# Kernel optimization log

Measured on AMD Instinct MI355X. Metric: run time of the kernel, lower is better.

Reference implementation:

```python
import jax, jax.numpy as jnp
import numpy as np

NUM_HEADS = 6
WS = 3

def setup_inputs() -> dict:
    key = jax.random.key(0)
    k1, k2, k3 = jax.random.split(key, 3)
    dim = 192
    x = jax.random.normal(k1, (2, dim, 48, 48, 48), dtype=jnp.float32)
    Wqkv = jax.random.normal(k2, (3 * dim, dim), dtype=jnp.float32) * (dim ** -0.5)
    Wproj = jax.random.normal(k3, (dim, dim), dtype=jnp.float32) * (dim ** -0.5)
    bproj = jnp.zeros((dim,), dtype=jnp.float32)
    return {"x": x, "Wqkv": Wqkv, "Wproj": Wproj, "bproj": bproj, "H": 384, "W": 288}

def reference(x, Wqkv, Wproj, bproj, H, W):
    b, c, h, w, d = x.shape
    xt = x.reshape(b, -1, c)                      # (B, N, C) with C = c, N = h*w*d
    B, N, C = xt.shape
    nh, ws = NUM_HEADS, WS
    hd = C // nh
    scale = hd ** -0.5
    hg, wg = H // ws, W // ws
    tg = hg * wg
    # window partition: (B, hg, ws, wg, ws, C) -> (B, hg, wg, ws, ws, C)
    xw = xt.reshape(B, hg, ws, wg, ws, C).transpose(0, 1, 3, 2, 4, 5)
    # fused QKV projection (no bias)
    qkv = jnp.einsum('bgvijc,oc->bgvijo', xw, Wqkv)          # (B,hg,wg,ws,ws,3C)
    qkv = qkv.reshape(B, tg, ws * ws, 3, nh, hd).transpose(3, 0, 1, 4, 2, 5)
    q, k, v = qkv[0], qkv[1], qkv[2]                          # (B, tg, nh, 9, hd)
    attn = jnp.einsum('bgnqd,bgnkd->bgnqk', q, k) * scale     # (B, tg, nh, 9, 9)
    attn = jax.nn.softmax(attn, axis=-1)
    out = jnp.einsum('bgnqk,bgnkd->bgnqd', attn, v)           # (B, tg, nh, 9, hd)
    out = out.transpose(0, 1, 3, 2, 4).reshape(B, hg, wg, ws, ws, C)
    out = jnp.swapaxes(out, 2, 3).reshape(B, N, C)            # un-window
    out = out @ Wproj.T + bproj
    return out.reshape(b, c, h, w, d)
```

## Files before the change

kernel.cpp:

```cpp
#include <hip/hip_runtime.h>

typedef _Float16 f16;
typedef _Float16 f16x4 __attribute__((ext_vector_type(4)));
typedef _Float16 f16x8 __attribute__((ext_vector_type(8)));
typedef float f32x4 __attribute__((ext_vector_type(4)));

#define TPB  576
#define NWIN 16
#define XS   200
#define WSS  200
#define QS   40
#define VS   264

#define WSQF_HALVES 110592
#define WS_NEEDED   (221184 + 73728)

__global__ __launch_bounds__(512) void conv_w(
    const float* __restrict__ Wqkv, const float* __restrict__ Wproj,
    f16* __restrict__ wsWqf, f16* __restrict__ wsWpf)
{
    int idx = blockIdx.x * 512 + threadIdx.x;
    if (idx < WSQF_HALVES) {
        int h    = idx / 18432;
        int rem  = idx % 18432;
        int ct   = rem / 3072;
        int rem2 = rem % 3072;
        int kk   = rem2 / 512;
        int rem3 = rem2 % 512;
        int lane = rem3 / 8;
        int e    = rem3 % 8;
        int r    = 16 * ct + (lane & 15);
        int grow = (r >> 5) * 192 + h * 32 + (r & 31);
        int col  = kk * 32 + (lane >> 4) * 8 + e;
        wsWqf[idx] = (f16)Wqkv[grow * 192 + col];
    } else {
        int j    = idx - WSQF_HALVES;
        int h    = j / 6144;
        int rem  = j % 6144;
        int nt   = rem / 512;
        int rem2 = rem % 512;
        int lane = rem2 / 8;
        int e    = rem2 % 8;
        wsWpf[j] = (f16)Wproj[(16 * nt + (lane & 15)) * 192 + h * 32 + (lane >> 4) * 8 + e];
    }
}

__global__ __launch_bounds__(TPB) void lsa_mfma11(
    const float* __restrict__ x, const f16* __restrict__ wsWqf,
    const f16* __restrict__ wsWpf, const float* __restrict__ bproj,
    float* __restrict__ out)
{
    __shared__ __attribute__((aligned(16))) f16 Xh[144 * XS];
    __shared__ __attribute__((aligned(16))) f16 Qh[144 * QS];
    __shared__ __attribute__((aligned(16))) f16 Kh[144 * QS];
    __shared__ __attribute__((aligned(16))) f16 Vt2[32 * VS];
    __shared__ __attribute__((aligned(16))) f16 AOh[144 * QS];

    const int tid  = threadIdx.x;
    const int lane = tid & 63;
    const int w    = tid >> 6;
    const int ci   = w / 3;
    const int ti   = w % 3;
    const int l15  = lane & 15;
    const int lg   = lane >> 4;

    const int  bb    = blockIdx.x / 768;
    const int  gbase = (blockIdx.x % 768) * NWIN;
    const long rb0   = (long)bb * 110592 + (long)(gbase / 96) * 864 + (long)(gbase % 96) * 3;

    const f16x8* wqf = (const f16x8*)wsWqf;
    const f16x8* wpf = (const f16x8*)wsWpf;

    for (int idx = tid; idx < 144 * 48; idx += TPB) {
        int t = idx / 48, c4 = idx % 48;
        int wi = t / 9, q = t - 9 * wi;
        long grow = rb0 + wi * 3 + (q / 3) * 288 + (q % 3);
        float4 xv = ((const float4*)x)[grow * 48 + c4];
        union { f16 h[4]; ushort4 u; } tmp;
        tmp.h[0] = (f16)xv.x; tmp.h[1] = (f16)xv.y; tmp.h[2] = (f16)xv.z; tmp.h[3] = (f16)xv.w;
        *(ushort4*)&Xh[t * XS + c4 * 4] = tmp.u;
    }
    {
        int4 z = {0, 0, 0, 0};
        for (int i2 = tid; i2 < (32 * VS * 2) / 16; i2 += TPB) ((int4*)Vt2)[i2] = z;
    }

    f32x4 pacc[3][4];
    #pragma unroll
    for (int a = 0; a < 3; ++a)
        #pragma unroll
        for (int bq = 0; bq < 4; ++bq)
            pacc[a][bq] = (f32x4){0.f, 0.f, 0.f, 0.f};

    __syncthreads();

    for (int h = 0; h < 6; ++h) {
        f32x4 qacc[2][3];
        #pragma unroll
        for (int c = 0; c < 2; ++c)
            #pragma unroll
            for (int t = 0; t < 3; ++t)
                qacc[c][t] = (f32x4){0.f, 0.f, 0.f, 0.f};
        #pragma unroll
        for (int kk = 0; kk < 6; ++kk) {
            f16x8 af[2], bf[3];
            af[0] = wqf[((h * 6 + ci    ) * 6 + kk) * 64 + lane];
            af[1] = wqf[((h * 6 + ci + 3) * 6 + kk) * 64 + lane];
            #pragma unroll
            for (int t = 0; t < 3; ++t)
                bf[t] = *(const f16x8*)&Xh[(16 * (ti + 3 * t) + l15) * XS + kk * 32 + lg * 8];
            #pragma unroll
            for (int c = 0; c < 2; ++c)
                #pragma unroll
                for (int t = 0; t < 3; ++t)
                    qacc[c][t] = __builtin_amdgcn_mfma_f32_16x16x32_f16(af[c], bf[t], qacc[c][t], 0, 0, 0);
        }
        #pragma unroll
        for (int c = 0; c < 2; ++c) {
            const int ct = ci + 3 * c;
            #pragma unroll
            for (int t = 0; t < 3; ++t) {
                const int token = 16 * (ti + 3 * t) + l15;
                f16x4 ph;
                ph[0] = (f16)qacc[c][t][0]; ph[1] = (f16)qacc[c][t][1];
                ph[2] = (f16)qacc[c][t][2]; ph[3] = (f16)qacc[c][t][3];
                if (ct < 2) {
                    *(f16x4*)&Qh[token * QS + ct * 16 + 4 * lg] = ph;
                } else if (ct < 4) {
                    *(f16x4*)&Kh[token * QS + (ct - 2) * 16 + 4 * lg] = ph;
                } else {
                    const int d0 = (ct - 4) * 16 + 4 * lg;
                    int wi = token / 9, qq = token - 9 * wi;
                    #pragma unroll
                    for (int r = 0; r < 4; ++r)
                        Vt2[(d0 + r) * VS + 16 * wi + qq] = ph[r];
                }
            }
        }
        __syncthreads();

        for (int wi = w; wi < NWIN; wi += 9) {
            int krow = 9 * wi + l15;
            krow = krow > 143 ? 143 : krow;
            f16x8 ak = *(const f16x8*)&Kh[krow * QS + lg * 8];
            f16x8 aq = *(const f16x8*)&Qh[krow * QS + lg * 8];
            f32x4 s = (f32x4){0.f, 0.f, 0.f, 0.f};
            s = __builtin_amdgcn_mfma_f32_16x16x32_f16(ak, aq, s, 0, 0, 0);
            float lgt[4];
            float mx = -1e30f;
            #pragma unroll
            for (int r = 0; r < 4; ++r) {
                int kx = 4 * lg + r;
                lgt[r] = (kx < 9) ? s[r] * 0.17677669529663687f : -1e30f;
                mx = fmaxf(mx, lgt[r]);
            }
            mx = fmaxf(mx, __shfl_xor(mx, 16));
            mx = fmaxf(mx, __shfl_xor(mx, 32));
            float e[4], sum = 0.f;
            #pragma unroll
            for (int r = 0; r < 4; ++r) {
                int kx = 4 * lg + r;
                e[r] = (kx < 9) ? __expf(lgt[r] - mx) : 0.f;
                sum += e[r];
            }
            sum += __shfl_xor(sum, 16);
            sum += __shfl_xor(sum, 32);
            float inv = 1.0f / sum;
            f16x4 p;
            p[0] = (f16)(e[0] * inv); p[1] = (f16)(e[1] * inv);
            p[2] = (f16)(e[2] * inv); p[3] = (f16)(e[3] * inv);
            #pragma unroll
            for (int dt = 0; dt < 2; ++dt) {
                f16x4 av = *(const f16x4*)&Vt2[(dt * 16 + l15) * VS + 16 * wi + 4 * lg];
                f32x4 o = (f32x4){0.f, 0.f, 0.f, 0.f};
                o = __builtin_amdgcn_mfma_f32_16x16x16f16(av, p, o, 0, 0, 0);
                if (l15 < 9) {
                    f16x4 oh;
                    oh[0] = (f16)o[0]; oh[1] = (f16)o[1]; oh[2] = (f16)o[2]; oh[3] = (f16)o[3];
                    *(f16x4*)&AOh[(9 * wi + l15) * QS + dt * 16 + 4 * lg] = oh;
                }
            }
        }
        __syncthreads();

        {
            f16x8 bw[4];
            #pragma unroll
            for (int bq = 0; bq < 4; ++bq)
                bw[bq] = wpf[(h * 12 + 4 * ti + bq) * 64 + lane];
            f16x8 aof[3];
            #pragma unroll
            for (int a = 0; a < 3; ++a)
                aof[a] = *(const f16x8*)&AOh[(16 * (3 * ci + a) + l15) * QS + lg * 8];
            #pragma unroll
            for (int bq = 0; bq < 4; ++bq)
                #pragma unroll
                for (int a = 0; a < 3; ++a)
                    pacc[a][bq] = __builtin_amdgcn_mfma_f32_16x16x32_f16(aof[a], bw[bq], pacc[a][bq], 0, 0, 0);
        }
    }

    float bv[4];
    #pragma unroll
    for (int bq = 0; bq < 4; ++bq)
        bv[bq] = bproj[16 * (4 * ti + bq) + l15];
    #pragma unroll
    for (int a = 0; a < 3; ++a) {
        #pragma unroll
        for (int r = 0; r < 4; ++r) {
            int t = 16 * (3 * ci + a) + lg * 4 + r;
            int wi = t / 9, q = t - 9 * wi;
            long grow = rb0 + wi * 3 + (q / 3) * 288 + (q % 3);
            float* dst = out + grow * 192;
            #pragma unroll
            for (int bq = 0; bq < 4; ++bq)
                dst[16 * (4 * ti + bq) + l15] = pacc[a][bq][r] + bv[bq];
        }
    }
}

__global__ __launch_bounds__(TPB) void lsa_mfma7(
    const float* __restrict__ x, const float* __restrict__ Wqkv,
    const float* __restrict__ Wproj, const float* __restrict__ bproj,
    float* __restrict__ out)
{
    __shared__ f16 Xh[144 * XS];
    __shared__ f16 Wh[96 * WSS];
    __shared__ f16 Qh[144 * QS];
    __shared__ f16 Kh[144 * QS];
    __shared__ f16 Vt2[32 * VS];
    __shared__ f16 AOh[144 * QS];
    __shared__ f16 Wp[192 * QS];

    const int tid  = threadIdx.x;
    const int lane = tid & 63;
    const int w    = tid >> 6;
    const int ci   = w / 3;
    const int ti   = w % 3;
    const int l15  = lane & 15;
    const int lg   = lane >> 4;

    const int  bb    = blockIdx.x / 768;
    const int  gbase = (blockIdx.x % 768) * NWIN;
    const long rb0   = (long)bb * 110592 + (long)(gbase / 96) * 864 + (long)(gbase % 96) * 3;

    const float4* Wq4 = (const float4*)Wqkv;
    const float4* Wp4 = (const float4*)Wproj;

    for (int idx = tid; idx < 144 * 48; idx += TPB) {
        int t = idx / 48, c4 = idx % 48;
        int wi = t / 9, q = t - 9 * wi;
        long grow = rb0 + wi * 3 + (q / 3) * 288 + (q % 3);
        float4 xv = ((const float4*)x)[grow * 48 + c4];
        union { f16 h[4]; ushort4 u; } tmp;
        tmp.h[0] = (f16)xv.x; tmp.h[1] = (f16)xv.y; tmp.h[2] = (f16)xv.z; tmp.h[3] = (f16)xv.w;
        *(ushort4*)&Xh[t * XS + c4 * 4] = tmp.u;
    }
    {
        int4 z = {0, 0, 0, 0};
        for (int i2 = tid; i2 < (32 * VS * 2) / 16; i2 += TPB) ((int4*)Vt2)[i2] = z;
    }
    #pragma unroll
    for (int i = 0; i < 8; ++i) {
        int l = i * TPB + tid;
        int r = l / 48, c4 = l % 48;
        float4 wv = Wq4[((r >> 5) * 192 + (r & 31)) * 48 + c4];
        union { f16 h4[4]; ushort4 u; } t;
        t.h4[0] = (f16)wv.x; t.h4[1] = (f16)wv.y; t.h4[2] = (f16)wv.z; t.h4[3] = (f16)wv.w;
        *(ushort4*)&Wh[r * WSS + c4 * 4] = t.u;
    }

    f32x4 pacc[3][4];
    #pragma unroll
    for (int a = 0; a < 3; ++a)
        #pragma unroll
        for (int bq = 0; bq < 4; ++bq)
            pacc[a][bq] = (f32x4){0.f, 0.f, 0.f, 0.f};

    __syncthreads();

    for (int h = 0; h < 6; ++h) {
        f32x4 qacc[2][3];
        #pragma unroll
        for (int c = 0; c < 2; ++c)
            #pragma unroll
            for (int t = 0; t < 3; ++t)
                qacc[c][t] = (f32x4){0.f, 0.f, 0.f, 0.f};
        #pragma unroll
        for (int kk = 0; kk < 6; ++kk) {
            f16x8 af[2], bf[3];
            #pragma unroll
            for (int c = 0; c < 2; ++c)
                af[c] = *(const f16x8*)&Wh[(16 * (ci + 3 * c) + l15) * WSS + kk * 32 + lg * 8];
            #pragma unroll
            for (int t = 0; t < 3; ++t)
                bf[t] = *(const f16x8*)&Xh[(16 * (ti + 3 * t) + l15) * XS + kk * 32 + lg * 8];
            #pragma unroll
            for (int c = 0; c < 2; ++c)
                #pragma unroll
                for (int t = 0; t < 3; ++t)
                    qacc[c][t] = __builtin_amdgcn_mfma_f32_16x16x32_f16(af[c], bf[t], qacc[c][t], 0, 0, 0);
        }
        #pragma unroll
        for (int c = 0; c < 2; ++c) {
            const int ct = ci + 3 * c;
            #pragma unroll
            for (int t = 0; t < 3; ++t) {
                const int token = 16 * (ti + 3 * t) + l15;
                f16x4 ph;
                ph[0] = (f16)qacc[c][t][0]; ph[1] = (f16)qacc[c][t][1];
                ph[2] = (f16)qacc[c][t][2]; ph[3] = (f16)qacc[c][t][3];
                if (ct < 2) {
                    *(f16x4*)&Qh[token * QS + ct * 16 + 4 * lg] = ph;
                } else if (ct < 4) {
                    *(f16x4*)&Kh[token * QS + (ct - 2) * 16 + 4 * lg] = ph;
                } else {
                    const int d0 = (ct - 4) * 16 + 4 * lg;
                    int wi = token / 9, qq = token - 9 * wi;
                    #pragma unroll
                    for (int r = 0; r < 4; ++r)
                        Vt2[(d0 + r) * VS + 16 * wi + qq] = ph[r];
                }
            }
        }
        __syncthreads();

        float4 wpv[3];
        if (tid < 512) {
            #pragma unroll
            for (int i = 0; i < 3; ++i) {
                int l = i * 512 + tid;
                int r = l / 8, c4 = l % 8;
                wpv[i] = Wp4[r * 48 + h * 8 + c4];
            }
        }
        if (h < 5) {
            #pragma unroll
            for (int i = 0; i < 8; ++i) {
                int l = i * TPB + tid;
                int r = l / 48, c4 = l % 48;
                float4 wv = Wq4[((r >> 5) * 192 + (h + 1) * 32 + (r & 31)) * 48 + c4];
                union { f16 h4[4]; ushort4 u; } t;
                t.h4[0] = (f16)wv.x; t.h4[1] = (f16)wv.y; t.h4[2] = (f16)wv.z; t.h4[3] = (f16)wv.w;
                *(ushort4*)&Wh[r * WSS + c4 * 4] = t.u;
            }
        }
        for (int wi = w; wi < NWIN; wi += 9) {
            int krow = 9 * wi + l15;
            krow = krow > 143 ? 143 : krow;
            f16x8 ak = *(const f16x8*)&Kh[krow * QS + lg * 8];
            f16x8 aq = *(const f16x8*)&Qh[krow * QS + lg * 8];
            f32x4 s = (f32x4){0.f, 0.f, 0.f, 0.f};
            s = __builtin_amdgcn_mfma_f32_16x16x32_f16(ak, aq, s, 0, 0, 0);
            float lgt[4];
            float mx = -1e30f;
            #pragma unroll
            for (int r = 0; r < 4; ++r) {
                int kx = 4 * lg + r;
                lgt[r] = (kx < 9) ? s[r] * 0.17677669529663687f : -1e30f;
                mx = fmaxf(mx, lgt[r]);
            }
            mx = fmaxf(mx, __shfl_xor(mx, 16));
            mx = fmaxf(mx, __shfl_xor(mx, 32));
            float e[4], sum = 0.f;
            #pragma unroll
            for (int r = 0; r < 4; ++r) {
                int kx = 4 * lg + r;
                e[r] = (kx < 9) ? __expf(lgt[r] - mx) : 0.f;
                sum += e[r];
            }
            sum += __shfl_xor(sum, 16);
            sum += __shfl_xor(sum, 32);
            float inv = 1.0f / sum;
            f16x4 p;
            p[0] = (f16)(e[0] * inv); p[1] = (f16)(e[1] * inv);
            p[2] = (f16)(e[2] * inv); p[3] = (f16)(e[3] * inv);
            #pragma unroll
            for (int dt = 0; dt < 2; ++dt) {
                f16x4 av = *(const f16x4*)&Vt2[(dt * 16 + l15) * VS + 16 * wi + 4 * lg];
                f32x4 o = (f32x4){0.f, 0.f, 0.f, 0.f};
                o = __builtin_amdgcn_mfma_f32_16x16x16f16(av, p, o, 0, 0, 0);
                if (l15 < 9) {
                    f16x4 oh;
                    oh[0] = (f16)o[0]; oh[1] = (f16)o[1]; oh[2] = (f16)o[2]; oh[3] = (f16)o[3];
                    *(f16x4*)&AOh[(9 * wi + l15) * QS + dt * 16 + 4 * lg] = oh;
                }
            }
        }
        if (tid < 512) {
            #pragma unroll
            for (int i = 0; i < 3; ++i) {
                int l = i * 512 + tid;
                int r = l / 8, c4 = l % 8;
                union { f16 h4[4]; ushort4 u; } t;
                t.h4[0] = (f16)wpv[i].x; t.h4[1] = (f16)wpv[i].y;
                t.h4[2] = (f16)wpv[i].z; t.h4[3] = (f16)wpv[i].w;
                *(ushort4*)&Wp[r * QS + c4 * 4] = t.u;
            }
        }
        __syncthreads();

        {
            f16x8 aof[3];
            #pragma unroll
            for (int a = 0; a < 3; ++a)
                aof[a] = *(const f16x8*)&AOh[(16 * (3 * ci + a) + l15) * QS + lg * 8];
            #pragma unroll
            for (int bq = 0; bq < 4; ++bq) {
                f16x8 bw = *(const f16x8*)&Wp[(16 * (4 * ti + bq) + l15) * QS + lg * 8];
                #pragma unroll
                for (int a = 0; a < 3; ++a)
                    pacc[a][bq] = __builtin_amdgcn_mfma_f32_16x16x32_f16(aof[a], bw, pacc[a][bq], 0, 0, 0);
            }
        }
    }

    float bv[4];
    #pragma unroll
    for (int bq = 0; bq < 4; ++bq)
        bv[bq] = bproj[16 * (4 * ti + bq) + l15];
    #pragma unroll
    for (int a = 0; a < 3; ++a) {
        #pragma unroll
        for (int r = 0; r < 4; ++r) {
            int t = 16 * (3 * ci + a) + lg * 4 + r;
            int wi = t / 9, q = t - 9 * wi;
            long grow = rb0 + wi * 3 + (q / 3) * 288 + (q % 3);
            float* dst = out + grow * 192;
            #pragma unroll
            for (int bq = 0; bq < 4; ++bq)
                dst[16 * (4 * ti + bq) + l15] = pacc[a][bq][r] + bv[bq];
        }
    }
}

extern "C" void kernel_launch(void* const* d_in, const int* in_sizes, int n_in,
                              void* d_out, int out_size, void* d_ws, size_t ws_size,
                              hipStream_t stream) {
    const float* x     = (const float*)d_in[0];
    const float* Wqkv  = (const float*)d_in[1];
    const float* Wproj = (const float*)d_in[2];
    const float* bproj = (const float*)d_in[3];
    float* out = (float*)d_out;
    if (ws_size >= (size_t)WS_NEEDED && d_ws != nullptr) {
        f16* wsWqf = (f16*)d_ws;
        f16* wsWpf = (f16*)((char*)d_ws + 221184);
        conv_w<<<288, 512, 0, stream>>>(Wqkv, Wproj, wsWqf, wsWpf);
        lsa_mfma11<<<1536, TPB, 0, stream>>>(x, wsWqf, wsWpf, bproj, out);
    } else {
        lsa_mfma7<<<1536, TPB, 0, stream>>>(x, Wqkv, Wproj, bproj, out);
    }
}
```

Baseline: 227.9 us.

## Process two heads per phase with double-buffered Q/K/V/AO to halve barriers

The fused windowed-attention kernel now computes QKV for two heads before each barrier, storing into duplicated shared buffers, then runs attention for 32 window-head items and two projection accumulations per phase. This halves the number of block-wide barriers and lets warps share attention work across heads. It raises LDS usage substantially and changes the V transpose stride from 264 to 260, which alters bank mapping. The fallback kernel gets its own V stride constant.

```diff
diff --git a/kernel.cpp b/kernel.cpp
--- a/kernel.cpp
+++ b/kernel.cpp
@@ -10,7 +10,8 @@
 #define XS   200
 #define WSS  200
 #define QS   40
-#define VS   264
+#define VS   260
+#define VSF  264
 
 #define WSQF_HALVES 110592
 #define WS_NEEDED   (221184 + 73728)
@@ -45,16 +46,16 @@
     }
 }
 
-__global__ __launch_bounds__(TPB) void lsa_mfma11(
+__global__ __launch_bounds__(TPB) void lsa_mfma12(
     const float* __restrict__ x, const f16* __restrict__ wsWqf,
     const f16* __restrict__ wsWpf, const float* __restrict__ bproj,
     float* __restrict__ out)
 {
     __shared__ __attribute__((aligned(16))) f16 Xh[144 * XS];
-    __shared__ __attribute__((aligned(16))) f16 Qh[144 * QS];
-    __shared__ __attribute__((aligned(16))) f16 Kh[144 * QS];
-    __shared__ __attribute__((aligned(16))) f16 Vt2[32 * VS];
-    __shared__ __attribute__((aligned(16))) f16 AOh[144 * QS];
+    __shared__ __attribute__((aligned(16))) f16 Qh2[2][144 * QS];
+    __shared__ __attribute__((aligned(16))) f16 Kh2[2][144 * QS];
+    __shared__ __attribute__((aligned(16))) f16 Vt2[2][32 * VS];
+    __shared__ __attribute__((aligned(16))) f16 AOh2[2][144 * QS];
 
     const int tid  = threadIdx.x;
     const int lane = tid & 63;
@@ -82,7 +83,7 @@
     }
     {
         int4 z = {0, 0, 0, 0};
-        for (int i2 = tid; i2 < (32 * VS * 2) / 16; i2 += TPB) ((int4*)Vt2)[i2] = z;
+        for (int i2 = tid; i2 < (2 * 32 * VS * 2) / 16; i2 += TPB) ((int4*)Vt2)[i2] = z;
     }
 
     f32x4 pacc[3][4];
@@ -94,6 +95,203 @@
 
     __syncthreads();
 
+    for (int p = 0; p < 3; ++p) {
+        #pragma unroll
+        for (int hh = 0; hh < 2; ++hh) {
+            const int h = 2 * p + hh;
+            f32x4 qacc[2][3];
+            #pragma unroll
+            for (int c = 0; c < 2; ++c)
+                #pragma unroll
+                for (int t = 0; t < 3; ++t)
+                    qacc[c][t] = (f32x4){0.f, 0.f, 0.f, 0.f};
+            #pragma unroll
+            for (int kk = 0; kk < 6; ++kk) {
+                f16x8 af[2], bf[3];
+                af[0] = wqf[((h * 6 + ci    ) * 6 + kk) * 64 + lane];
+                af[1] = wqf[((h * 6 + ci + 3) * 6 + kk) * 64 + lane];
+                #pragma unroll
+                for (int t = 0; t < 3; ++t)
+                    bf[t] = *(const f16x8*)&Xh[(16 * (ti + 3 * t) + l15) * XS + kk * 32 + lg * 8];
+                #pragma unroll
+                for (int c = 0; c < 2; ++c)
+                    #pragma unroll
+                    for (int t = 0; t < 3; ++t)
+                        qacc[c][t] = __builtin_amdgcn_mfma_f32_16x16x32_f16(af[c], bf[t], qacc[c][t], 0, 0, 0);
+            }
+            #pragma unroll
+            for (int c = 0; c < 2; ++c) {
+                const int ct = ci + 3 * c;
+                #pragma unroll
+                for (int t = 0; t < 3; ++t) {
+                    const int token = 16 * (ti + 3 * t) + l15;
+                    f16x4 ph;
+                    ph[0] = (f16)qacc[c][t][0]; ph[1] = (f16)qacc[c][t][1];
+                    ph[2] = (f16)qacc[c][t][2]; ph[3] = (f16)qacc[c][t][3];
+                    if (ct < 2) {
+                        *(f16x4*)&Qh2[hh][token * QS + ct * 16 + 4 * lg] = ph;
+                    } else if (ct < 4) {
+                        *(f16x4*)&Kh2[hh][token * QS + (ct - 2) * 16 + 4 * lg] = ph;
+                    } else {
+                        const int d0 = (ct - 4) * 16 + 4 * lg;
+                        int wi = token / 9, qq = token - 9 * wi;
+                        #pragma unroll
+                        for (int r = 0; r < 4; ++r)
+                            Vt2[hh][(d0 + r) * VS + 16 * wi + qq] = ph[r];
+                    }
+                }
+            }
+        }
+        __syncthreads();
+
+        for (int idx = w; idx < 32; idx += 9) {
+            const int hh = idx >> 4;
+            const int wi = idx & 15;
+            const f16* Qb = &Qh2[hh][0];
+            const f16* Kb = &Kh2[hh][0];
+            const f16* Vb = &Vt2[hh][0];
+            f16* Ab = &AOh2[hh][0];
+            int krow = 9 * wi + l15;
+            krow = krow > 143 ? 143 : krow;
+            f16x8 ak = *(const f16x8*)&Kb[krow * QS + lg * 8];
+            f16x8 aq = *(const f16x8*)&Qb[krow * QS + lg * 8];
+            f32x4 s = (f32x4){0.f, 0.f, 0.f, 0.f};
+            s = __builtin_amdgcn_mfma_f32_16x16x32_f16(ak, aq, s, 0, 0, 0);
+            float lgt[4];
+            float mx = -1e30f;
+            #pragma unroll
+            for (int r = 0; r < 4; ++r) {
+                int kx = 4 * lg + r;
+                lgt[r] = (kx < 9) ? s[r] * 0.17677669529663687f : -1e30f;
+                mx = fmaxf(mx, lgt[r]);
+            }
+            mx = fmaxf(mx, __shfl_xor(mx, 16));
+            mx = fmaxf(mx, __shfl_xor(mx, 32));
+            float e[4], sum = 0.f;
+            #pragma unroll
+            for (int r = 0; r < 4; ++r) {
+                int kx = 4 * lg + r;
+                e[r] = (kx < 9) ? __expf(lgt[r] - mx) : 0.f;
+                sum += e[r];
+            }
+            sum += __shfl_xor(sum, 16);
+            sum += __shfl_xor(sum, 32);
+            float inv = 1.0f / sum;
+            f16x4 pfrag;
+            pfrag[0] = (f16)(e[0] * inv); pfrag[1] = (f16)(e[1] * inv);
+            pfrag[2] = (f16)(e[2] * inv); pfrag[3] = (f16)(e[3] * inv);
+            #pragma unroll
+            for (int dt = 0; dt < 2; ++dt) {
+                f16x4 av = *(const f16x4*)&Vb[(dt * 16 + l15) * VS + 16 * wi + 4 * lg];
+                f32x4 o = (f32x4){0.f, 0.f, 0.f, 0.f};
+                o = __builtin_amdgcn_mfma_f32_16x16x16f16(av, pfrag, o, 0, 0, 0);
+                if (l15 < 9) {
+                    f16x4 oh;
+                    oh[0] = (f16)o[0]; oh[1] = (f16)o[1]; oh[2] = (f16)o[2]; oh[3] = (f16)o[3];
+                    *(f16x4*)&Ab[(9 * wi + l15) * QS + dt * 16 + 4 * lg] = oh;
+                }
+            }
+        }
+        __syncthreads();
+
+        #pragma unroll
+        for (int hh = 0; hh < 2; ++hh) {
+            const int h = 2 * p + hh;
+            f16x8 bw[4];
+            #pragma unroll
+            for (int bq = 0; bq < 4; ++bq)
+                bw[bq] = wpf[(h * 12 + 4 * ti + bq) * 64 + lane];
+            f16x8 aof[3];
+            #pragma unroll
+            for (int a = 0; a < 3; ++a)
+                aof[a] = *(const f16x8*)&AOh2[hh][(16 * (3 * ci + a) + l15) * QS + lg * 8];
+            #pragma unroll
+            for (int bq = 0; bq < 4; ++bq)
+                #pragma unroll
+                for (int a = 0; a < 3; ++a)
+                    pacc[a][bq] = __builtin_amdgcn_mfma_f32_16x16x32_f16(aof[a], bw[bq], pacc[a][bq], 0, 0, 0);
+        }
+    }
+
+    float bv[4];
+    #pragma unroll
+    for (int bq = 0; bq < 4; ++bq)
+        bv[bq] = bproj[16 * (4 * ti + bq) + l15];
+    #pragma unroll
+    for (int a = 0; a < 3; ++a) {
+        #pragma unroll
+        for (int r = 0; r < 4; ++r) {
+            int t = 16 * (3 * ci + a) + lg * 4 + r;
+            int wi = t / 9, q = t - 9 * wi;
+            long grow = rb0 + wi * 3 + (q / 3) * 288 + (q % 3);
+            float* dst = out + grow * 192;
+            #pragma unroll
+            for (int bq = 0; bq < 4; ++bq)
+                dst[16 * (4 * ti + bq) + l15] = pacc[a][bq][r] + bv[bq];
+        }
+    }
+}
+
+__global__ __launch_bounds__(TPB) void lsa_mfma7(
+    const float* __restrict__ x, const float* __restrict__ Wqkv,
+    const float* __restrict__ Wproj, const float* __restrict__ bproj,
+    float* __restrict__ out)
+{
+    __shared__ f16 Xh[144 * XS];
+    __shared__ f16 Wh[96 * WSS];
+    __shared__ f16 Qh[144 * QS];
+    __shared__ f16 Kh[144 * QS];
+    __shared__ f16 Vt2f[32 * VSF];
+    __shared__ f16 AOh[144 * QS];
+    __shared__ f16 Wp[192 * QS];
+
+    const int tid  = threadIdx.x;
+    const int lane = tid & 63;
+    const int w    = tid >> 6;
+    const int ci   = w / 3;
+    const int ti   = w % 3;
+    const int l15  = lane & 15;
+    const int lg   = lane >> 4;
+
+    const int  bb    = blockIdx.x / 768;
+    const int  gbase = (blockIdx.x % 768) * NWIN;
+    const long rb0   = (long)bb * 110592 + (long)(gbase / 96) * 864 + (long)(gbase % 96) * 3;
+
+    const float4* Wq4 = (const float4*)Wqkv;
+    const float4* Wp4 = (const float4*)Wproj;
+
+    for (int idx = tid; idx < 144 * 48; idx += TPB) {
+        int t = idx / 48, c4 = idx % 48;
+        int wi = t / 9, q = t - 9 * wi;
+        long grow = rb0 + wi * 3 + (q / 3) * 288 + (q % 3);
+        float4 xv = ((const float4*)x)[grow * 48 + c4];
+        union { f16 h[4]; ushort4 u; } tmp;
+        tmp.h[0] = (f16)xv.x; tmp.h[1] = (f16)xv.y; tmp.h[2] = (f16)xv.z; tmp.h[3] = (f16)xv.w;
+        *(ushort4*)&Xh[t * XS + c4 * 4] = tmp.u;
+    }
+    {
+        int4 z = {0, 0, 0, 0};
+        for (int i2 = tid; i2 < (32 * VSF * 2) / 16; i2 += TPB) ((int4*)Vt2f)[i2] = z;
+    }
+    #pragma unroll
+    for (int i = 0; i < 8; ++i) {
+        int l = i * TPB + tid;
+        int r = l / 48, c4 = l % 48;
+        float4 wv = Wq4[((r >> 5) * 192 + (r & 31)) * 48 + c4];
+        union { f16 h4[4]; ushort4 u; } t;
+        t.h4[0] = (f16)wv.x; t.h4[1] = (f16)wv.y; t.h4[2] = (f16)wv.z; t.h4[3] = (f16)wv.w;
+        *(ushort4*)&Wh[r * WSS + c4 * 4] = t.u;
+    }
+
+    f32x4 pacc[3][4];
+    #pragma unroll
+    for (int a = 0; a < 3; ++a)
+        #pragma unroll
+        for (int bq = 0; bq < 4; ++bq)
+            pacc[a][bq] = (f32x4){0.f, 0.f, 0.f, 0.f};
+
+    __syncthreads();
+
     for (int h = 0; h < 6; ++h) {
         f32x4 qacc[2][3];
         #pragma unroll
@@ -104,8 +302,9 @@
         #pragma unroll
         for (int kk = 0; kk < 6; ++kk) {
             f16x8 af[2], bf[3];
-            af[0] = wqf[((h * 6 + ci    ) * 6 + kk) * 64 + lane];
-            af[1] = wqf[((h * 6 + ci + 3) * 6 + kk) * 64 + lane];
+            #pragma unroll
+            for (int c = 0; c < 2; ++c)
+                af[c] = *(const f16x8*)&Wh[(16 * (ci + 3 * c) + l15) * WSS + kk * 32 + lg * 8];
             #pragma unroll
             for (int t = 0; t < 3; ++t)
                 bf[t] = *(const f16x8*)&Xh[(16 * (ti + 3 * t) + l15) * XS + kk * 32 + lg * 8];
@@ -133,12 +332,32 @@
                     int wi = token / 9, qq = token - 9 * wi;
                     #pragma unroll
                     for (int r = 0; r < 4; ++r)
-                        Vt2[(d0 + r) * VS + 16 * wi + qq] = ph[r];
+                        Vt2f[(d0 + r) * VSF + 16 * wi + qq] = ph[r];
                 }
             }
         }
         __syncthreads();
 
+        float4 wpv[3];
+        if (tid < 512) {
+            #pragma unroll
+            for (int i = 0; i < 3; ++i) {
+                int l = i * 512 + tid;
+                int r = l / 8, c4 = l % 8;
+                wpv[i] = Wp4[r * 48 + h * 8 + c4];
+            }
+        }
+        if (h < 5) {
+            #pragma unroll
+            for (int i = 0; i < 8; ++i) {
+                int l = i * TPB + tid;
+                int r = l / 48, c4 = l % 48;
+                float4 wv = Wq4[((r >> 5) * 192 + (h + 1) * 32 + (r & 31)) * 48 + c4];
+                union { f16 h4[4]; ushort4 u; } t;
+                t.h4[0] = (f16)wv.x; t.h4[1] = (f16)wv.y; t.h4[2] = (f16)wv.z; t.h4[3] = (f16)wv.w;
+                *(ushort4*)&Wh[r * WSS + c4 * 4] = t.u;
+            }
+        }
         for (int wi = w; wi < NWIN; wi += 9) {
             int krow = 9 * wi + l15;
             krow = krow > 143 ? 143 : krow;
@@ -166,220 +385,14 @@
             sum += __shfl_xor(sum, 16);
             sum += __shfl_xor(sum, 32);
             float inv = 1.0f / sum;
-            f16x4 p;
-            p[0] = (f16)(e[0] * inv); p[1] = (f16)(e[1] * inv);
-            p[2] = (f16)(e[2] * inv); p[3] = (f16)(e[3] * inv);
+            f16x4 pf;
+            pf[0] = (f16)(e[0] * inv); pf[1] = (f16)(e[1] * inv);
+            pf[2] = (f16)(e[2] * inv); pf[3] = (f16)(e[3] * inv);
             #pragma unroll
             for (int dt = 0; dt < 2; ++dt) {
-                f16x4 av = *(const f16x4*)&Vt2[(dt * 16 + l15) * VS + 16 * wi + 4 * lg];
+                f16x4 av = *(const f16x4*)&Vt2f[(dt * 16 + l15) * VSF + 16 * wi + 4 * lg];
                 f32x4 o = (f32x4){0.f, 0.f, 0.f, 0.f};
-                o = __builtin_amdgcn_mfma_f32_16x16x16f16(av, p, o, 0, 0, 0);
-                if (l15 < 9) {
-                    f16x4 oh;
-                    oh[0] = (f16)o[0]; oh[1] = (f16)o[1]; oh[2] = (f16)o[2]; oh[3] = (f16)o[3];
-                    *(f16x4*)&AOh[(9 * wi + l15) * QS + dt * 16 + 4 * lg] = oh;
-                }
-            }
-        }
-        __syncthreads();
-
-        {
-            f16x8 bw[4];
-            #pragma unroll
-            for (int bq = 0; bq < 4; ++bq)
-                bw[bq] = wpf[(h * 12 + 4 * ti + bq) * 64 + lane];
-            f16x8 aof[3];
-            #pragma unroll
-            for (int a = 0; a < 3; ++a)
-                aof[a] = *(const f16x8*)&AOh[(16 * (3 * ci + a) + l15) * QS + lg * 8];
-            #pragma unroll
-            for (int bq = 0; bq < 4; ++bq)
-                #pragma unroll
-                for (int a = 0; a < 3; ++a)
-                    pacc[a][bq] = __builtin_amdgcn_mfma_f32_16x16x32_f16(aof[a], bw[bq], pacc[a][bq], 0, 0, 0);
-        }
-    }
-
-    float bv[4];
-    #pragma unroll
-    for (int bq = 0; bq < 4; ++bq)
-        bv[bq] = bproj[16 * (4 * ti + bq) + l15];
-    #pragma unroll
-    for (int a = 0; a < 3; ++a) {
-        #pragma unroll
-        for (int r = 0; r < 4; ++r) {
-            int t = 16 * (3 * ci + a) + lg * 4 + r;
-            int wi = t / 9, q = t - 9 * wi;
-            long grow = rb0 + wi * 3 + (q / 3) * 288 + (q % 3);
-            float* dst = out + grow * 192;
-            #pragma unroll
-            for (int bq = 0; bq < 4; ++bq)
-                dst[16 * (4 * ti + bq) + l15] = pacc[a][bq][r] + bv[bq];
-        }
-    }
-}
-
-__global__ __launch_bounds__(TPB) void lsa_mfma7(
-    const float* __restrict__ x, const float* __restrict__ Wqkv,
-    const float* __restrict__ Wproj, const float* __restrict__ bproj,
-    float* __restrict__ out)
-{
-    __shared__ f16 Xh[144 * XS];
-    __shared__ f16 Wh[96 * WSS];
-    __shared__ f16 Qh[144 * QS];
-    __shared__ f16 Kh[144 * QS];
-    __shared__ f16 Vt2[32 * VS];
-    __shared__ f16 AOh[144 * QS];
-    __shared__ f16 Wp[192 * QS];
-
-    const int tid  = threadIdx.x;
-    const int lane = tid & 63;
-    const int w    = tid >> 6;
-    const int ci   = w / 3;
-    const int ti   = w % 3;
-    const int l15  = lane & 15;
-    const int lg   = lane >> 4;
-
-    const int  bb    = blockIdx.x / 768;
-    const int  gbase = (blockIdx.x % 768) * NWIN;
-    const long rb0   = (long)bb * 110592 + (long)(gbase / 96) * 864 + (long)(gbase % 96) * 3;
-
-    const float4* Wq4 = (const float4*)Wqkv;
-    const float4* Wp4 = (const float4*)Wproj;
-
-    for (int idx = tid; idx < 144 * 48; idx += TPB) {
-        int t = idx / 48, c4 = idx % 48;
-        int wi = t / 9, q = t - 9 * wi;
-        long grow = rb0 + wi * 3 + (q / 3) * 288 + (q % 3);
-        float4 xv = ((const float4*)x)[grow * 48 + c4];
-        union { f16 h[4]; ushort4 u; } tmp;
-        tmp.h[0] = (f16)xv.x; tmp.h[1] = (f16)xv.y; tmp.h[2] = (f16)xv.z; tmp.h[3] = (f16)xv.w;
-        *(ushort4*)&Xh[t * XS + c4 * 4] = tmp.u;
-    }
-    {
-        int4 z = {0, 0, 0, 0};
-        for (int i2 = tid; i2 < (32 * VS * 2) / 16; i2 += TPB) ((int4*)Vt2)[i2] = z;
-    }
-    #pragma unroll
-    for (int i = 0; i < 8; ++i) {
-        int l = i * TPB + tid;
-        int r = l / 48, c4 = l % 48;
-        float4 wv = Wq4[((r >> 5) * 192 + (r & 31)) * 48 + c4];
-        union { f16 h4[4]; ushort4 u; } t;
-        t.h4[0] = (f16)wv.x; t.h4[1] = (f16)wv.y; t.h4[2] = (f16)wv.z; t.h4[3] = (f16)wv.w;
-        *(ushort4*)&Wh[r * WSS + c4 * 4] = t.u;
-    }
-
-    f32x4 pacc[3][4];
-    #pragma unroll
-    for (int a = 0; a < 3; ++a)
-        #pragma unroll
-        for (int bq = 0; bq < 4; ++bq)
-            pacc[a][bq] = (f32x4){0.f, 0.f, 0.f, 0.f};
-
-    __syncthreads();
-
-    for (int h = 0; h < 6; ++h) {
-        f32x4 qacc[2][3];
-        #pragma unroll
-        for (int c = 0; c < 2; ++c)
-            #pragma unroll
-            for (int t = 0; t < 3; ++t)
-                qacc[c][t] = (f32x4){0.f, 0.f, 0.f, 0.f};
-        #pragma unroll
-        for (int kk = 0; kk < 6; ++kk) {
-            f16x8 af[2], bf[3];
-            #pragma unroll
-            for (int c = 0; c < 2; ++c)
-                af[c] = *(const f16x8*)&Wh[(16 * (ci + 3 * c) + l15) * WSS + kk * 32 + lg * 8];
-            #pragma unroll
-            for (int t = 0; t < 3; ++t)
-                bf[t] = *(const f16x8*)&Xh[(16 * (ti + 3 * t) + l15) * XS + kk * 32 + lg * 8];
-            #pragma unroll
-            for (int c = 0; c < 2; ++c)
-                #pragma unroll
-                for (int t = 0; t < 3; ++t)
-                    qacc[c][t] = __builtin_amdgcn_mfma_f32_16x16x32_f16(af[c], bf[t], qacc[c][t], 0, 0, 0);
-        }
-        #pragma unroll
-        for (int c = 0; c < 2; ++c) {
-            const int ct = ci + 3 * c;
-            #pragma unroll
-            for (int t = 0; t < 3; ++t) {
-                const int token = 16 * (ti + 3 * t) + l15;
-                f16x4 ph;
-                ph[0] = (f16)qacc[c][t][0]; ph[1] = (f16)qacc[c][t][1];
-                ph[2] = (f16)qacc[c][t][2]; ph[3] = (f16)qacc[c][t][3];
-                if (ct < 2) {
-                    *(f16x4*)&Qh[token * QS + ct * 16 + 4 * lg] = ph;
-                } else if (ct < 4) {
-                    *(f16x4*)&Kh[token * QS + (ct - 2) * 16 + 4 * lg] = ph;
-                } else {
-                    const int d0 = (ct - 4) * 16 + 4 * lg;
-                    int wi = token / 9, qq = token - 9 * wi;
-                    #pragma unroll
-                    for (int r = 0; r < 4; ++r)
-                        Vt2[(d0 + r) * VS + 16 * wi + qq] = ph[r];
-                }
-            }
-        }
-        __syncthreads();
-
-        float4 wpv[3];
-        if (tid < 512) {
-            #pragma unroll
-            for (int i = 0; i < 3; ++i) {
-                int l = i * 512 + tid;
-                int r = l / 8, c4 = l % 8;
-                wpv[i] = Wp4[r * 48 + h * 8 + c4];
-            }
-        }
-        if (h < 5) {
-            #pragma unroll
-            for (int i = 0; i < 8; ++i) {
-                int l = i * TPB + tid;
-                int r = l / 48, c4 = l % 48;
-                float4 wv = Wq4[((r >> 5) * 192 + (h + 1) * 32 + (r & 31)) * 48 + c4];
-                union { f16 h4[4]; ushort4 u; } t;
-                t.h4[0] = (f16)wv.x; t.h4[1] = (f16)wv.y; t.h4[2] = (f16)wv.z; t.h4[3] = (f16)wv.w;
-                *(ushort4*)&Wh[r * WSS + c4 * 4] = t.u;
-            }
-        }
-        for (int wi = w; wi < NWIN; wi += 9) {
-            int krow = 9 * wi + l15;
-            krow = krow > 143 ? 143 : krow;
-            f16x8 ak = *(const f16x8*)&Kh[krow * QS + lg * 8];
-            f16x8 aq = *(const f16x8*)&Qh[krow * QS + lg * 8];
-            f32x4 s = (f32x4){0.f, 0.f, 0.f, 0.f};
-            s = __builtin_amdgcn_mfma_f32_16x16x32_f16(ak, aq, s, 0, 0, 0);
-            float lgt[4];
-            float mx = -1e30f;
-            #pragma unroll
-            for (int r = 0; r < 4; ++r) {
-                int kx = 4 * lg + r;
-                lgt[r] = (kx < 9) ? s[r] * 0.17677669529663687f : -1e30f;
-                mx = fmaxf(mx, lgt[r]);
-            }
-            mx = fmaxf(mx, __shfl_xor(mx, 16));
-            mx = fmaxf(mx, __shfl_xor(mx, 32));
-            float e[4], sum = 0.f;
-            #pragma unroll
-            for (int r = 0; r < 4; ++r) {
-                int kx = 4 * lg + r;
-                e[r] = (kx < 9) ? __expf(lgt[r] - mx) : 0.f;
-                sum += e[r];
-            }
-            sum += __shfl_xor(sum, 16);
-            sum += __shfl_xor(sum, 32);
-            float inv = 1.0f / sum;
-            f16x4 p;
-            p[0] = (f16)(e[0] * inv); p[1] = (f16)(e[1] * inv);
-            p[2] = (f16)(e[2] * inv); p[3] = (f16)(e[3] * inv);
-            #pragma unroll
-            for (int dt = 0; dt < 2; ++dt) {
-                f16x4 av = *(const f16x4*)&Vt2[(dt * 16 + l15) * VS + 16 * wi + 4 * lg];
-                f32x4 o = (f32x4){0.f, 0.f, 0.f, 0.f};
-                o = __builtin_amdgcn_mfma_f32_16x16x16f16(av, p, o, 0, 0, 0);
+                o = __builtin_amdgcn_mfma_f32_16x16x16f16(av, pf, o, 0, 0, 0);
                 if (l15 < 9) {
                     f16x4 oh;
                     oh[0] = (f16)o[0]; oh[1] = (f16)o[1]; oh[2] = (f16)o[2]; oh[3] = (f16)o[3];
@@ -446,7 +459,7 @@
         f16* wsWqf = (f16*)d_ws;
         f16* wsWpf = (f16*)((char*)d_ws + 221184);
         conv_w<<<288, 512, 0, stream>>>(Wqkv, Wproj, wsWqf, wsWpf);
-        lsa_mfma11<<<1536, TPB, 0, stream>>>(x, wsWqf, wsWpf, bproj, out);
+        lsa_mfma12<<<1536, TPB, 0, stream>>>(x, wsWqf, wsWpf, bproj, out);
     } else {
         lsa_mfma7<<<1536, TPB, 0, stream>>>(x, Wqkv, Wproj, bproj, out);
     }
```

After: 221.8 us. 2.7% less time.
